# Kernel tuning notes

Measured on AMD Instinct MI355X. Metric: run time of the kernel, lower is better.

The kernel has to match this reference:

```python
import jax, jax.numpy as jnp
import numpy as np

B, A, M = 64, 128, 8          # batch (conformers), atoms, ensemble models
D, O0, O2, O4, O6 = 384, 256, 192, 160, 1  # AEV dim and padded layer out dims


def setup_inputs() -> dict:
    key = jax.random.key(0)
    ks = jax.random.split(key, 10)
    return {
        "species": jax.random.randint(ks[0], (B, A), 0, 4),
        "aev": jax.random.normal(ks[1], (B, A, D), dtype=jnp.float32),
        "w0": jax.random.normal(ks[2], (1, A, M, O0, D), dtype=jnp.float32),
        "b0": jax.random.normal(ks[3], (1, A, M, O0, 1), dtype=jnp.float32),
        "w2": jax.random.normal(ks[4], (1, A, M, O2, O0), dtype=jnp.float32),
        "b2": jax.random.normal(ks[5], (1, A, M, O2, 1), dtype=jnp.float32),
        "w4": jax.random.normal(ks[6], (1, A, M, O4, O2), dtype=jnp.float32),
        "b4": jax.random.normal(ks[7], (1, A, M, O4, 1), dtype=jnp.float32),
        "w6": jax.random.normal(ks[8], (1, A, M, O6, O4), dtype=jnp.float32),
        "b6": jax.random.normal(ks[9], (1, A, M, O6, 1), dtype=jnp.float32),
    }


def _celu(x, alpha=0.1):
    # F.celu(x, alpha) = max(0,x) + min(0, alpha*(exp(x/alpha)-1))
    return jnp.where(x > 0, x, alpha * jnp.expm1(x / alpha))


def reference(species, aev, w0, b0, w2, b2, w4, b4, w6, b6):
    # batchedLinear(v, W, b) == W @ v + b per (atom, model) block,
    # broadcast over batch; first layer broadcasts the model dim (1 -> M).
    # x: [B, A, M, out]
    x = jnp.einsum('zamoi,bai->bamo', w0, aev) + b0[..., 0]
    x = _celu(x)
    x = jnp.einsum('zamoi,bami->bamo', w2, x) + b2[..., 0]
    x = _celu(x)
    x = jnp.einsum('zamoi,bami->bamo', w4, x) + b4[..., 0]
    x = _celu(x)
    x = jnp.einsum('zamoi,bami->bamo', w6, x) + b6[..., 0]
    # sum over atoms, models, out (and the trailing singleton), divide by n_models
    energies = jnp.sum(x, axis=(1, 2, 3)) / M  # [B]
    return species, energies
```

## Files before the change

kernel.cpp:

```cpp
#include <hip/hip_runtime.h>

#define B_ 64
#define A_ 128
#define M_ 8
#define D_ 384
#define O0_ 256
#define O2_ 192
#define O4_ 160

typedef float f32x4 __attribute__((ext_vector_type(4)));
typedef _Float16 f16x8 __attribute__((ext_vector_type(8)));
typedef _Float16 f16x4 __attribute__((ext_vector_type(4)));

__device__ __forceinline__ float celu_f(float x) {
    return x > 0.f ? x : 0.1f * (__expf(x * 10.f) - 1.f);
}

__device__ __forceinline__ f32x4 zero4() {
    f32x4 v; v[0] = 0.f; v[1] = 0.f; v[2] = 0.f; v[3] = 0.f; return v;
}

template<int K, int O, int OPITCH, bool SWZ_OUT>
__device__ __forceinline__ void layer_mfma(const float* __restrict__ W,
                                           const float* __restrict__ bias,
                                           const _Float16* Xin, _Float16* Xout,
                                           int wave, int col, int quad)
{
    constexpr int KSTEPS = K / 32;
    constexpr int OTILES = O / 16;
    for (int ot = wave; ot < OTILES; ot += 8) {
        const float* wrow = W + (size_t)(ot * 16 + col) * K + quad * 8;
        f32x4 acc[4];
        #pragma unroll
        for (int nt = 0; nt < 4; ++nt) acc[nt] = zero4();
        #pragma unroll
        for (int ks = 0; ks < KSTEPS; ++ks) {
            f32x4 wlo = *(const f32x4*)(wrow + ks * 32);
            f32x4 whi = *(const f32x4*)(wrow + ks * 32 + 4);
            f16x8 afr;
            afr[0] = (_Float16)wlo[0]; afr[1] = (_Float16)wlo[1];
            afr[2] = (_Float16)wlo[2]; afr[3] = (_Float16)wlo[3];
            afr[4] = (_Float16)whi[0]; afr[5] = (_Float16)whi[1];
            afr[6] = (_Float16)whi[2]; afr[7] = (_Float16)whi[3];
            #pragma unroll
            for (int nt = 0; nt < 4; ++nt) {
                const int b = nt * 16 + col;
                const int c = ks * 4 + quad;
                const f16x8 bfr = *(const f16x8*)(Xin + b * K + ((c ^ (b & 7)) * 8));
                acc[nt] = __builtin_amdgcn_mfma_f32_16x16x32_f16(afr, bfr, acc[nt], 0, 0, 0);
            }
        }
        const f32x4 bias4 = *(const f32x4*)(bias + ot * 16 + quad * 4);
        const int o0 = ot * 16 + quad * 4;
        #pragma unroll
        for (int nt = 0; nt < 4; ++nt) {
            const int b = nt * 16 + col;
            f16x4 h;
            #pragma unroll
            for (int r = 0; r < 4; ++r) h[r] = (_Float16)celu_f(acc[nt][r] + bias4[r]);
            if (SWZ_OUT) {
                const int c = o0 >> 3;
                *(f16x4*)(Xout + b * OPITCH + ((c ^ (b & 7)) * 8) + (o0 & 7)) = h;
            } else {
                *(f16x4*)(Xout + b * OPITCH + o0) = h;
            }
        }
    }
}

__global__ __launch_bounds__(512, 4) void nn_kernel(
    const float* __restrict__ aev,
    const float* __restrict__ w0, const float* __restrict__ b0,
    const float* __restrict__ w2, const float* __restrict__ b2,
    const float* __restrict__ w4, const float* __restrict__ b4,
    const float* __restrict__ w6, const float* __restrict__ b6,
    float* __restrict__ out)
{
    __shared__ __align__(16) unsigned char smem_raw[57344];
    _Float16* const lds = (_Float16*)smem_raw;

    const int tid  = threadIdx.x;
    const int wave = tid >> 6;
    const int lane = tid & 63;
    const int col  = lane & 15;
    const int quad = lane >> 4;

    const int a  = blockIdx.x & 127;
    const int m  = blockIdx.x >> 7;
    const int am = a * 8 + m;

    const float* w0p = w0 + (size_t)am * O0_ * D_;
    const float* b0p = b0 + am * O0_;
    const float* w2p = w2 + (size_t)am * O2_ * O0_;
    const float* b2p = b2 + am * O2_;
    const float* w4p = w4 + (size_t)am * O4_ * O2_;
    const float* b4p = b4 + am * O4_;
    const float* w6p = w6 + am * O4_;
    const float  b6v = b6[am];

    _Float16* bufStage = lds;
    _Float16* X0 = lds + 12288;
    _Float16* X2 = lds;
    _Float16* X4 = lds + 12288;
    float* part = (float*)(smem_raw + 45568);

    f32x4 acc0[2][4];
    #pragma unroll
    for (int i = 0; i < 2; ++i)
        #pragma unroll
        for (int nt = 0; nt < 4; ++nt) acc0[i][nt] = zero4();

    #pragma unroll
    for (int kc = 0; kc < 2; ++kc) {
        if (kc) __syncthreads();
        #pragma unroll
        for (int it = 0; it < 3; ++it) {
            const int idx = tid + it * 512;
            const int b = idx / 24;
            const int c = idx % 24;
            const float* src = aev + ((size_t)b * A_ + a) * D_ + kc * 192 + c * 8;
            f32x4 lo = *(const f32x4*)src;
            f32x4 hi = *(const f32x4*)(src + 4);
            f16x8 h;
            h[0] = (_Float16)lo[0]; h[1] = (_Float16)lo[1];
            h[2] = (_Float16)lo[2]; h[3] = (_Float16)lo[3];
            h[4] = (_Float16)hi[0]; h[5] = (_Float16)hi[1];
            h[6] = (_Float16)hi[2]; h[7] = (_Float16)hi[3];
            *(f16x8*)(bufStage + b * 192 + ((c ^ (b & 7)) * 8)) = h;
        }
        __syncthreads();
        #pragma unroll
        for (int i = 0; i < 2; ++i) {
            const int ot = wave + i * 8;
            const float* wrow = w0p + (size_t)(ot * 16 + col) * D_ + kc * 192 + quad * 8;
            #pragma unroll
            for (int ks = 0; ks < 6; ++ks) {
                f32x4 wlo = *(const f32x4*)(wrow + ks * 32);
                f32x4 whi = *(const f32x4*)(wrow + ks * 32 + 4);
                f16x8 afr;
                afr[0] = (_Float16)wlo[0]; afr[1] = (_Float16)wlo[1];
                afr[2] = (_Float16)wlo[2]; afr[3] = (_Float16)wlo[3];
                afr[4] = (_Float16)whi[0]; afr[5] = (_Float16)whi[1];
                afr[6] = (_Float16)whi[2]; afr[7] = (_Float16)whi[3];
                #pragma unroll
                for (int nt = 0; nt < 4; ++nt) {
                    const int b = nt * 16 + col;
                    const int c = ks * 4 + quad;
                    const f16x8 bfr = *(const f16x8*)(bufStage + b * 192 + ((c ^ (b & 7)) * 8));
                    acc0[i][nt] = __builtin_amdgcn_mfma_f32_16x16x32_f16(afr, bfr, acc0[i][nt], 0, 0, 0);
                }
            }
        }
    }
    #pragma unroll
    for (int i = 0; i < 2; ++i) {
        const int ot = wave + i * 8;
        const f32x4 bias4 = *(const f32x4*)(b0p + ot * 16 + quad * 4);
        const int o0 = ot * 16 + quad * 4;
        #pragma unroll
        for (int nt = 0; nt < 4; ++nt) {
            const int b = nt * 16 + col;
            f16x4 h;
            #pragma unroll
            for (int r = 0; r < 4; ++r) h[r] = (_Float16)celu_f(acc0[i][nt][r] + bias4[r]);
            const int c = o0 >> 3;
            *(f16x4*)(X0 + b * 256 + ((c ^ (b & 7)) * 8) + (o0 & 7)) = h;
        }
    }
    __syncthreads();

    layer_mfma<256, 192, 192, true>(w2p, b2p, X0, X2, wave, col, quad);
    __syncthreads();

    layer_mfma<192, 160, 164, false>(w4p, b4p, X2, X4, wave, col, quad);
    __syncthreads();

    {
        const int b  = tid & 63;
        const int pt = tid >> 6;
        const _Float16* xrow = X4 + b * 164 + pt * 20;
        const float* wseg = w6p + pt * 20;
        float s = 0.f;
        #pragma unroll
        for (int j = 0; j < 5; ++j) {
            f32x4 wv = *(const f32x4*)(wseg + j * 4);
            f16x4 xv = *(const f16x4*)(xrow + j * 4);
            s += wv[0] * (float)xv[0] + wv[1] * (float)xv[1] +
                 wv[2] * (float)xv[2] + wv[3] * (float)xv[3];
        }
        part[tid] = s;
    }
    __syncthreads();
    if (tid < 64) {
        float x6 = b6v;
        #pragma unroll
        for (int p = 0; p < 8; ++p) x6 += part[tid + 64 * p];
        atomicAdd(out + B_ * A_ + tid, x6 * 0.125f);
    }
}

__global__ void init_out_kernel(const int* __restrict__ species, float* __restrict__ out) {
    const int i = blockIdx.x * 256 + threadIdx.x;
    if (i < B_ * A_) out[i] = (float)species[i];
    if (i < B_) out[B_ * A_ + i] = 0.f;
}

extern "C" void kernel_launch(void* const* d_in, const int* in_sizes, int n_in,
                              void* d_out, int out_size, void* d_ws, size_t ws_size,
                              hipStream_t stream) {
    const int*   species = (const int*)d_in[0];
    const float* aev = (const float*)d_in[1];
    const float* w0  = (const float*)d_in[2];
    const float* b0  = (const float*)d_in[3];
    const float* w2  = (const float*)d_in[4];
    const float* b2  = (const float*)d_in[5];
    const float* w4  = (const float*)d_in[6];
    const float* b4  = (const float*)d_in[7];
    const float* w6  = (const float*)d_in[8];
    const float* b6  = (const float*)d_in[9];
    float* out = (float*)d_out;

    hipLaunchKernelGGL(init_out_kernel, dim3(32), dim3(256), 0, stream, species, out);
    hipLaunchKernelGGL(nn_kernel, dim3(A_ * M_), dim3(512), 0, stream,
                       aev, w0, b0, w2, b2, w4, b4, w6, b6, out);
}
```

Measured before the change: 749.3 us.

## Stage weight panels into LDS via global_load_lds and remap waves to output tiles

Weights for each layer are no longer read straight from global memory into registers. Each layer now copies 32-row panels of fp32 weights into a swizzled LDS buffer using the direct global-to-LDS load builtin, then all waves read their A fragments from that panel. Work is also split differently: each wave owns one batch tile and one half of the panel's output rows, instead of one output tile across all four batch tiles. The aim is fully coalesced weight fetches and fewer redundant per-lane global loads. The cost is a single-buffered design with two barriers per panel and no overlap between loading and MFMA work, plus LDS growing to 80KB, which may reduce resident blocks.

```diff
diff --git a/kernel.cpp b/kernel.cpp
--- a/kernel.cpp
+++ b/kernel.cpp
@@ -20,53 +20,55 @@
     f32x4 v; v[0] = 0.f; v[1] = 0.f; v[2] = 0.f; v[3] = 0.f; return v;
 }
 
-template<int K, int O, int OPITCH, bool SWZ_OUT>
-__device__ __forceinline__ void layer_mfma(const float* __restrict__ W,
-                                           const float* __restrict__ bias,
-                                           const _Float16* Xin, _Float16* Xout,
-                                           int wave, int col, int quad)
+#define GLOAD_LDS16(gp, lp)                                                     \
+    __builtin_amdgcn_global_load_lds(                                           \
+        (const __attribute__((address_space(1))) void*)(gp),                    \
+        (__attribute__((address_space(3))) void*)(lp), 16, 0, 0)
+
+template<int K, int KH>
+__device__ __forceinline__ void stage_panel(const float* __restrict__ W,
+                                            int row0, int col0,
+                                            unsigned char* panelBase,
+                                            int wave, int lane)
 {
-    constexpr int KSTEPS = K / 32;
-    constexpr int OTILES = O / 16;
-    for (int ot = wave; ot < OTILES; ot += 8) {
-        const float* wrow = W + (size_t)(ot * 16 + col) * K + quad * 8;
-        f32x4 acc[4];
-        #pragma unroll
-        for (int nt = 0; nt < 4; ++nt) acc[nt] = zero4();
-        #pragma unroll
-        for (int ks = 0; ks < KSTEPS; ++ks) {
-            f32x4 wlo = *(const f32x4*)(wrow + ks * 32);
-            f32x4 whi = *(const f32x4*)(wrow + ks * 32 + 4);
-            f16x8 afr;
-            afr[0] = (_Float16)wlo[0]; afr[1] = (_Float16)wlo[1];
-            afr[2] = (_Float16)wlo[2]; afr[3] = (_Float16)wlo[3];
-            afr[4] = (_Float16)whi[0]; afr[5] = (_Float16)whi[1];
-            afr[6] = (_Float16)whi[2]; afr[7] = (_Float16)whi[3];
-            #pragma unroll
-            for (int nt = 0; nt < 4; ++nt) {
-                const int b = nt * 16 + col;
-                const int c = ks * 4 + quad;
-                const f16x8 bfr = *(const f16x8*)(Xin + b * K + ((c ^ (b & 7)) * 8));
-                acc[nt] = __builtin_amdgcn_mfma_f32_16x16x32_f16(afr, bfr, acc[nt], 0, 0, 0);
-            }
-        }
-        const f32x4 bias4 = *(const f32x4*)(bias + ot * 16 + quad * 4);
-        const int o0 = ot * 16 + quad * 4;
-        #pragma unroll
-        for (int nt = 0; nt < 4; ++nt) {
-            const int b = nt * 16 + col;
-            f16x4 h;
-            #pragma unroll
-            for (int r = 0; r < 4; ++r) h[r] = (_Float16)celu_f(acc[nt][r] + bias4[r]);
-            if (SWZ_OUT) {
-                const int c = o0 >> 3;
-                *(f16x4*)(Xout + b * OPITCH + ((c ^ (b & 7)) * 8) + (o0 & 7)) = h;
-            } else {
-                *(f16x4*)(Xout + b * OPITCH + o0) = h;
-            }
-        }
-    }
-}
+    constexpr int CPR   = KH / 4;
+    constexpr int CALLS = (32 * KH * 4) / (1024 * 8);
+    #pragma unroll
+    for (int j = 0; j < CALLS; ++j) {
+        const int cb = (wave * CALLS + j);
+        const int C  = cb * 64 + lane;
+        const int r  = C / CPR;
+        const int q  = C % CPR;
+        const int gq = q ^ (r & 7);
+        const float* src = W + (size_t)(row0 + r) * K + col0 + gq * 4;
+        GLOAD_LDS16(src, panelBase + cb * 1024);
+    }
+}
+
+template<int KH>
+__device__ __forceinline__ f16x8 read_afrag(const unsigned char* panelBase,
+                                            int rr, int ksl, int quad)
+{
+    const float* row = (const float*)(panelBase + rr * (KH * 4));
+    const int q0 = quad * 2 + ksl * 8;
+    const f32x4 lo = *(const f32x4*)(row + ((q0 ^ (rr & 7)) * 4));
+    const f32x4 hi = *(const f32x4*)(row + (((q0 + 1) ^ (rr & 7)) * 4));
+    f16x8 a;
+    a[0] = (_Float16)lo[0]; a[1] = (_Float16)lo[1];
+    a[2] = (_Float16)lo[2]; a[3] = (_Float16)lo[3];
+    a[4] = (_Float16)hi[0]; a[5] = (_Float16)hi[1];
+    a[6] = (_Float16)hi[2]; a[7] = (_Float16)hi[3];
+    return a;
+}
+
+#define AEVBUF_OFF 0
+#define PANEL0_OFF 24576
+#define X0_OFF     49152
+#define X2_OFF     0
+#define PANEL2_OFF 24576
+#define X4_OFF     24576
+#define PANEL4_OFF 49152
+#define PART_OFF   45568
 
 __global__ __launch_bounds__(512, 4) void nn_kernel(
     const float* __restrict__ aev,
@@ -76,14 +78,16 @@
     const float* __restrict__ w6, const float* __restrict__ b6,
     float* __restrict__ out)
 {
-    __shared__ __align__(16) unsigned char smem_raw[57344];
-    _Float16* const lds = (_Float16*)smem_raw;
+    __shared__ __align__(16) unsigned char smem_raw[81920];
 
     const int tid  = threadIdx.x;
     const int wave = tid >> 6;
     const int lane = tid & 63;
     const int col  = lane & 15;
     const int quad = lane >> 4;
+    const int tb   = wave >> 2;
+    const int nt   = wave & 3;
+    const int brow = nt * 16 + col;
 
     const int a  = blockIdx.x & 127;
     const int m  = blockIdx.x >> 7;
@@ -98,21 +102,19 @@
     const float* w6p = w6 + am * O4_;
     const float  b6v = b6[am];
 
-    _Float16* bufStage = lds;
-    _Float16* X0 = lds + 12288;
-    _Float16* X2 = lds;
-    _Float16* X4 = lds + 12288;
-    float* part = (float*)(smem_raw + 45568);
-
-    f32x4 acc0[2][4];
-    #pragma unroll
-    for (int i = 0; i < 2; ++i)
-        #pragma unroll
-        for (int nt = 0; nt < 4; ++nt) acc0[i][nt] = zero4();
+    _Float16* aevbuf = (_Float16*)(smem_raw + AEVBUF_OFF);
+    _Float16* X0     = (_Float16*)(smem_raw + X0_OFF);
+    _Float16* X2     = (_Float16*)(smem_raw + X2_OFF);
+    _Float16* X4     = (_Float16*)(smem_raw + X4_OFF);
+    float*    part   = (float*)(smem_raw + PART_OFF);
+
+    f32x4 acc0[8];
+    #pragma unroll
+    for (int op = 0; op < 8; ++op) acc0[op] = zero4();
 
     #pragma unroll
     for (int kc = 0; kc < 2; ++kc) {
-        if (kc) __syncthreads();
+        __syncthreads();
         #pragma unroll
         for (int it = 0; it < 3; ++it) {
             const int idx = tid + it * 512;
@@ -126,53 +128,90 @@
             h[2] = (_Float16)lo[2]; h[3] = (_Float16)lo[3];
             h[4] = (_Float16)hi[0]; h[5] = (_Float16)hi[1];
             h[6] = (_Float16)hi[2]; h[7] = (_Float16)hi[3];
-            *(f16x8*)(bufStage + b * 192 + ((c ^ (b & 7)) * 8)) = h;
-        }
+            *(f16x8*)(aevbuf + b * 192 + ((c ^ (b & 7)) * 8)) = h;
+        }
+        #pragma unroll
+        for (int op = 0; op < 8; ++op) {
+            __syncthreads();
+            stage_panel<D_, 192>(w0p, op * 32, kc * 192,
+                                 smem_raw + PANEL0_OFF, wave, lane);
+            __syncthreads();
+            const int rr = tb * 16 + col;
+            #pragma unroll
+            for (int ksl = 0; ksl < 6; ++ksl) {
+                const f16x8 af = read_afrag<192>(smem_raw + PANEL0_OFF, rr, ksl, quad);
+                const int c = (quad + ksl * 4) ^ (brow & 7);
+                const f16x8 bf = *(const f16x8*)(aevbuf + brow * 192 + c * 8);
+                acc0[op] = __builtin_amdgcn_mfma_f32_16x16x32_f16(af, bf, acc0[op], 0, 0, 0);
+            }
+        }
+    }
+    #pragma unroll
+    for (int op = 0; op < 8; ++op) {
+        const int tile = op * 2 + tb;
+        const int o0 = tile * 16 + quad * 4;
+        const f32x4 bias4 = *(const f32x4*)(b0p + o0);
+        f16x4 h;
+        #pragma unroll
+        for (int r = 0; r < 4; ++r) h[r] = (_Float16)celu_f(acc0[op][r] + bias4[r]);
+        const int c = o0 >> 3;
+        *(f16x4*)(X0 + brow * 256 + ((c ^ (brow & 7)) * 8) + (o0 & 7)) = h;
+    }
+    __syncthreads();
+
+    #pragma unroll
+    for (int op = 0; op < 6; ++op) {
+        f32x4 acc = zero4();
+        #pragma unroll
+        for (int kc = 0; kc < 2; ++kc) {
+            __syncthreads();
+            stage_panel<O0_, 128>(w2p, op * 32, kc * 128,
+                                  smem_raw + PANEL2_OFF, wave, lane);
+            __syncthreads();
+            const int rr = tb * 16 + col;
+            #pragma unroll
+            for (int ksl = 0; ksl < 4; ++ksl) {
+                const f16x8 af = read_afrag<128>(smem_raw + PANEL2_OFF, rr, ksl, quad);
+                const int ksg = kc * 4 + ksl;
+                const int c = (quad + ksg * 4) ^ (brow & 7);
+                const f16x8 bf = *(const f16x8*)(X0 + brow * 256 + c * 8);
+                acc = __builtin_amdgcn_mfma_f32_16x16x32_f16(af, bf, acc, 0, 0, 0);
+            }
+        }
+        const int tile = op * 2 + tb;
+        const int o0 = tile * 16 + quad * 4;
+        const f32x4 bias4 = *(const f32x4*)(b2p + o0);
+        f16x4 h;
+        #pragma unroll
+        for (int r = 0; r < 4; ++r) h[r] = (_Float16)celu_f(acc[r] + bias4[r]);
+        const int c = o0 >> 3;
+        *(f16x4*)(X2 + brow * 192 + ((c ^ (brow & 7)) * 8) + (o0 & 7)) = h;
+    }
+    __syncthreads();
+
+    #pragma unroll
+    for (int op = 0; op < 5; ++op) {
+        f32x4 acc = zero4();
         __syncthreads();
-        #pragma unroll
-        for (int i = 0; i < 2; ++i) {
-            const int ot = wave + i * 8;
-            const float* wrow = w0p + (size_t)(ot * 16 + col) * D_ + kc * 192 + quad * 8;
-            #pragma unroll
-            for (int ks = 0; ks < 6; ++ks) {
-                f32x4 wlo = *(const f32x4*)(wrow + ks * 32);
-                f32x4 whi = *(const f32x4*)(wrow + ks * 32 + 4);
-                f16x8 afr;
-                afr[0] = (_Float16)wlo[0]; afr[1] = (_Float16)wlo[1];
-                afr[2] = (_Float16)wlo[2]; afr[3] = (_Float16)wlo[3];
-                afr[4] = (_Float16)whi[0]; afr[5] = (_Float16)whi[1];
-                afr[6] = (_Float16)whi[2]; afr[7] = (_Float16)whi[3];
-                #pragma unroll
-                for (int nt = 0; nt < 4; ++nt) {
-                    const int b = nt * 16 + col;
-                    const int c = ks * 4 + quad;
-                    const f16x8 bfr = *(const f16x8*)(bufStage + b * 192 + ((c ^ (b & 7)) * 8));
-                    acc0[i][nt] = __builtin_amdgcn_mfma_f32_16x16x32_f16(afr, bfr, acc0[i][nt], 0, 0, 0);
-                }
-            }
-        }
-    }
-    #pragma unroll
-    for (int i = 0; i < 2; ++i) {
-        const int ot = wave + i * 8;
-        const f32x4 bias4 = *(const f32x4*)(b0p + ot * 16 + quad * 4);
-        const int o0 = ot * 16 + quad * 4;
-        #pragma unroll
-        for (int nt = 0; nt < 4; ++nt) {
-            const int b = nt * 16 + col;
-            f16x4 h;
-            #pragma unroll
-            for (int r = 0; r < 4; ++r) h[r] = (_Float16)celu_f(acc0[i][nt][r] + bias4[r]);
-            const int c = o0 >> 3;
-            *(f16x4*)(X0 + b * 256 + ((c ^ (b & 7)) * 8) + (o0 & 7)) = h;
-        }
-    }
-    __syncthreads();
-
-    layer_mfma<256, 192, 192, true>(w2p, b2p, X0, X2, wave, col, quad);
-    __syncthreads();
-
-    layer_mfma<192, 160, 164, false>(w4p, b4p, X2, X4, wave, col, quad);
+        stage_panel<O2_, 192>(w4p, op * 32, 0,
+                              smem_raw + PANEL4_OFF, wave, lane);
+        __syncthreads();
+        const int rr = tb * 16 + col;
+        #pragma unroll
+        for (int ksl = 0; ksl < 6; ++ksl) {
+            const f16x8 af = read_afrag<192>(smem_raw + PANEL4_OFF, rr, ksl, quad);
+            const int c = (quad + ksl * 4) ^ (brow & 7);
+            const f16x8 bf = *(const f16x8*)(X2 + brow * 192 + c * 8);
+            acc = __builtin_amdgcn_mfma_f32_16x16x32_f16(af, bf, acc, 0, 0, 0);
+        }
+        const int tile = op * 2 + tb;
+        const int o0 = tile * 16 + quad * 4;
+        const f32x4 bias4 = *(const f32x4*)(b4p + o0);
+        f16x4 h;
+        #pragma unroll
+        for (int r = 0; r < 4; ++r) h[r] = (_Float16)celu_f(acc[r] + bias4[r]);
+        *(f16x4*)(X4 + brow * 164 + o0) = h;
+    }
     __syncthreads();
 
     {
```

Measured after the change: 735.1 us. About the same (-1.9%).
